# Optimization experiments

Hardware: AMD Instinct MI355X
Metric: run time of the kernel (lower is better)

## Reference

```python
import jax, jax.numpy as jnp
import numpy as np

B, T, N = 8, 100, 100000
MARGIN = 0.1
THRESHOLD = 0.5
BIG = 1.0e9


def setup_inputs() -> dict:
    key = jax.random.key(0)
    k0, k1, k2, k3, k4 = jax.random.split(key, 5)
    outputs = jax.random.normal(k0, (B, T, 3), dtype=jnp.float32)
    c2ws = jax.random.normal(k1, (B, 4, 4), dtype=jnp.float32)
    scene_scales = jax.random.uniform(k2, (B,), dtype=jnp.float32)
    means = jax.random.normal(k3, (N, 3), dtype=jnp.float32)
    scales = jax.random.uniform(k4, (N, 3), dtype=jnp.float32)
    return {"outputs": outputs, "c2ws": c2ws, "scene_scales": scene_scales,
            "means": means, "scales": scales}


def reference(outputs, c2ws, scene_scales, means, scales):
    # per-splat max radius (precomputed in torch __init__)
    maxsplatrad = jnp.max(scales, axis=1)                      # [N]
    # world transform: aff = R * scene_scale, trans = translation
    aff = c2ws[:, :3, :3] * scene_scales[:, None, None]        # [B,3,3]
    trans = c2ws[:, :3, 3]                                     # [B,3]
    # baddbmm(trans, outputs, aff.mT) == outputs @ aff^T + trans
    retrajs = jnp.einsum('btd,bed->bte', outputs, aff) + trans[:, None, :]  # [B,T,3]
    # axis-aligned bbox of each trajectory, expanded by threshold
    thres = THRESHOLD * scene_scales[0]
    uvals = jnp.max(retrajs, axis=1) + thres                   # [B,3]
    lvals = jnp.min(retrajs, axis=1) - thres                   # [B,3]
    # bbox filter: which splats fall inside each trajectory bbox
    inside = jnp.all((means[None, :, :] >= lvals[:, None, :]) &
                     (means[None, :, :] <= uvals[:, None, :]), axis=2)  # [B,N]
    # pairwise distances via ||a-b||^2 = |a|^2 + |b|^2 - 2 a.b (avoids [B,T,N,3])
    r2 = jnp.sum(retrajs * retrajs, axis=-1)                   # [B,T]
    m2 = jnp.sum(means * means, axis=-1)                       # [N]
    cross = jnp.einsum('btd,nd->btn', retrajs, means)          # [B,T,N]
    d2 = r2[:, :, None] + m2[None, None, :] - 2.0 * cross
    dist = jnp.sqrt(jnp.maximum(d2, 0.0))
    resdists = dist - maxsplatrad[None, None, :] - MARGIN      # [B,T,N]
    # scatter_reduce amin with include_self=False and 1e9 default ==
    # masked min over splats; pairs not inside bbox never scattered -> BIG
    masked = jnp.where(inside[:, None, :], resdists, BIG)
    collosses = jnp.min(masked, axis=2)                        # [B,T]
    return jnp.sum(jax.nn.relu(-collosses)) / (B * T)
```

## Files before the change

### kernel.cpp

```cpp
#include <hip/hip_runtime.h>

constexpr int   B_ = 8;
constexpr int   T_ = 100;
constexpr int   NPAIRS = B_ * T_;
constexpr int   N_ = 100000;
constexpr float MARGIN_ = 0.1f;
constexpr float THRESHOLD_ = 0.5f;
constexpr float BIG_ = 1000000000.0f;

constexpr size_t PM_OFF     = 0;
constexpr size_t MSR_OFF    = PM_OFF + (size_t)N_ * 16;
constexpr size_t KEYS_OFF   = MSR_OFF + (size_t)N_ * 32;
constexpr size_t PAIRS_OFF  = KEYS_OFF + 4096;
constexpr size_t BOUNDS_OFF = PAIRS_OFF + 16384;

__device__ __forceinline__ float fsqrt(float x) { return __builtin_amdgcn_sqrtf(x); }

__device__ __forceinline__ unsigned fkey(float f) {
    unsigned u = __float_as_uint(f);
    return (u & 0x80000000u) ? ~u : (u | 0x80000000u);
}

__global__ void k_prep(const float* __restrict__ outputs,
                       const float* __restrict__ c2ws,
                       const float* __restrict__ ss,
                       char* ws) {
    __shared__ float re_s[NPAIRS * 3];
    int tid = threadIdx.x;
    float4*   pairs  = (float4*)(ws + PAIRS_OFF);
    float*    bounds = (float*)(ws + BOUNDS_OFF);
    unsigned* keys   = (unsigned*)(ws + KEYS_OFF);

    if (tid < NPAIRS) {
        int b = tid / T_;
        float s = ss[b];
        const float* o = outputs + tid * 3;
        float o0 = o[0], o1 = o[1], o2 = o[2];
        const float* c = c2ws + b * 16;
        float re[3];
#pragma unroll
        for (int e = 0; e < 3; e++) {
            re[e] = (o0 * c[e * 4 + 0] + o1 * c[e * 4 + 1] + o2 * c[e * 4 + 2]) * s + c[e * 4 + 3];
            re_s[tid * 3 + e] = re[e];
        }
        pairs[tid] = make_float4(re[0], re[1], re[2], 0.f);
        keys[tid] = fkey(BIG_);
    }

    __syncthreads();
    if (tid < 24) {
        int b = tid / 3, e = tid - b * 3;
        float mx = -3.4e38f, mn = 3.4e38f;
        for (int t = 0; t < T_; t++) {
            float v = re_s[(b * T_ + t) * 3 + e];
            mx = fmaxf(mx, v);
            mn = fminf(mn, v);
        }
        float thres = THRESHOLD_ * ss[0];
        bounds[b * 3 + e]      = mn - thres;
        bounds[24 + b * 3 + e] = mx + thres;
    }
}

__global__ void k_means(const float* __restrict__ means,
                        const float* __restrict__ scales,
                        char* ws) {
    int n = blockIdx.x * blockDim.x + threadIdx.x;
    if (n >= N_) return;
    const float* bounds = (const float*)(ws + BOUNDS_OFF);
    float4* pm   = (float4*)(ws + PM_OFF);
    float4* msrv = (float4*)(ws + MSR_OFF);

    float mx = means[n * 3 + 0], my = means[n * 3 + 1], mz = means[n * 3 + 2];
    float msr = fmaxf(fmaxf(scales[n * 3 + 0], scales[n * 3 + 1]), scales[n * 3 + 2]) + MARGIN_;
    float eff[8];
#pragma unroll
    for (int b = 0; b < 8; b++) {
        bool in = (mx >= bounds[b * 3 + 0]) & (mx <= bounds[24 + b * 3 + 0]) &
                  (my >= bounds[b * 3 + 1]) & (my <= bounds[24 + b * 3 + 1]) &
                  (mz >= bounds[b * 3 + 2]) & (mz <= bounds[24 + b * 3 + 2]);
        eff[b] = in ? msr : -BIG_;
    }
    pm[n] = make_float4(mx, my, mz, 0.f);
    msrv[n * 2 + 0] = make_float4(eff[0], eff[1], eff[2], eff[3]);
    msrv[n * 2 + 1] = make_float4(eff[4], eff[5], eff[6], eff[7]);
}

constexpr int PER = 98;
constexpr int NBLK = (N_ + PER - 1) / PER;

__global__ __launch_bounds__(256) void k_main(const char* __restrict__ wsc, char* ws) {
    __shared__ float4 pm_s[PER];
    __shared__ float  msr_s[PER * 8];
    int tid = threadIdx.x;
    const float4* pmg   = (const float4*)(wsc + PM_OFF);
    const float4* msrg  = (const float4*)(wsc + MSR_OFF);
    const float4* pairs = (const float4*)(wsc + PAIRS_OFF);
    unsigned* keys = (unsigned*)(ws + KEYS_OFF);

    int base = blockIdx.x * PER;
    int cnt  = min(PER, N_ - base);

    if (tid < cnt) pm_s[tid] = pmg[base + tid];
    if (tid < 2 * cnt) ((float4*)msr_s)[tid] = msrg[2 * base + tid];

    int p0 = tid, p1 = tid + 256, p2 = tid + 512;
    float4 q0 = pairs[p0];
    float4 q1 = pairs[p1];
    float4 q2 = pairs[p2];
    int b0 = p0 / T_, b1 = p1 / T_, b2 = p2 / T_;

    __syncthreads();

    float mn0 = BIG_, mn1 = BIG_, mn2 = BIG_;
    const float*  mp = msr_s;
    const float4* sp = pm_s;
    for (int i = 0; i < cnt; i++) {
        float4 m = sp[i];
        float e0 = mp[b0], e1 = mp[b1], e2 = mp[b2];
        mp += 8;
        float dx, dy, dz, d2;
        dx = q0.x - m.x; dy = q0.y - m.y; dz = q0.z - m.z;
        d2 = fmaf(dz, dz, fmaf(dy, dy, dx * dx));
        mn0 = fminf(mn0, fsqrt(d2) - e0);
        dx = q1.x - m.x; dy = q1.y - m.y; dz = q1.z - m.z;
        d2 = fmaf(dz, dz, fmaf(dy, dy, dx * dx));
        mn1 = fminf(mn1, fsqrt(d2) - e1);
        dx = q2.x - m.x; dy = q2.y - m.y; dz = q2.z - m.z;
        d2 = fmaf(dz, dz, fmaf(dy, dy, dx * dx));
        mn2 = fminf(mn2, fsqrt(d2) - e2);
    }
    atomicMin(&keys[p0], fkey(mn0));
    atomicMin(&keys[p1], fkey(mn1));
    atomicMin(&keys[p2], fkey(mn2));

    if (tid < 32) {
        int p3 = 768 + tid;
        float4 q3 = pairs[p3];
        int b3 = p3 / T_;
        float mn3 = BIG_;
        const float* mp3 = msr_s;
        for (int i = 0; i < cnt; i++) {
            float4 m = pm_s[i];
            float e3 = mp3[b3];
            mp3 += 8;
            float dx = q3.x - m.x, dy = q3.y - m.y, dz = q3.z - m.z;
            float d2 = fmaf(dz, dz, fmaf(dy, dy, dx * dx));
            mn3 = fminf(mn3, fsqrt(d2) - e3);
        }
        atomicMin(&keys[p3], fkey(mn3));
    }
}

__global__ void k_final(const char* __restrict__ wsc, float* __restrict__ out) {
    const unsigned* keys = (const unsigned*)(wsc + KEYS_OFF);
    int tid = threadIdx.x;
    float acc = 0.f;
    for (int p = tid; p < NPAIRS; p += 256) {
        unsigned k = keys[p];
        unsigned u = (k & 0x80000000u) ? (k ^ 0x80000000u) : ~k;
        float f = __uint_as_float(u);
        acc += fmaxf(0.f, -f);
    }
#pragma unroll
    for (int off = 32; off; off >>= 1) acc += __shfl_down(acc, off, 64);
    __shared__ float wsum[4];
    if ((tid & 63) == 0) wsum[tid >> 6] = acc;
    __syncthreads();
    if (tid == 0) out[0] = (wsum[0] + wsum[1] + wsum[2] + wsum[3]) / (float)(B_ * T_);
}

extern "C" void kernel_launch(void* const* d_in, const int* in_sizes, int n_in,
                              void* d_out, int out_size, void* d_ws, size_t ws_size,
                              hipStream_t stream) {
    const float* outputs = (const float*)d_in[0];
    const float* c2ws    = (const float*)d_in[1];
    const float* ss      = (const float*)d_in[2];
    const float* means   = (const float*)d_in[3];
    const float* scales  = (const float*)d_in[4];
    float* out = (float*)d_out;
    char*  ws  = (char*)d_ws;

    hipLaunchKernelGGL(k_prep, dim3(1), dim3(1024), 0, stream, outputs, c2ws, ss, ws);
    hipLaunchKernelGGL(k_means, dim3((N_ + 255) / 256), dim3(256), 0, stream, means, scales, ws);
    hipLaunchKernelGGL(k_main, dim3(NBLK), dim3(256), 0, stream, (const char*)ws, ws);
    hipLaunchKernelGGL(k_final, dim3(1), dim3(256), 0, stream, (const char*)ws, out);
}
```

Before: 101.5 us.

## Fuse means preprocessing and final reduction into main kernel

Removes the separate per-splat preprocessing kernel by computing bbox masks and max radii directly into shared memory in the main kernel. Replaces the final reduction kernel with a last-block-done pattern using an atomic counter and threadfences. This cuts two kernel launches and the global round trip of the preprocessed splat arrays. The cost is an extra atomic and fence per block, plus redundant bound loads per thread.

```diff
diff --git a/kernel.cpp b/kernel.cpp
--- a/kernel.cpp
+++ b/kernel.cpp
@@ -8,11 +8,10 @@
 constexpr float THRESHOLD_ = 0.5f;
 constexpr float BIG_ = 1000000000.0f;
 
-constexpr size_t PM_OFF     = 0;
-constexpr size_t MSR_OFF    = PM_OFF + (size_t)N_ * 16;
-constexpr size_t KEYS_OFF   = MSR_OFF + (size_t)N_ * 32;
-constexpr size_t PAIRS_OFF  = KEYS_OFF + 4096;
-constexpr size_t BOUNDS_OFF = PAIRS_OFF + 16384;
+constexpr size_t PAIRS_OFF  = 0;
+constexpr size_t BOUNDS_OFF = 16384;
+constexpr size_t KEYS_OFF   = BOUNDS_OFF + 256;
+constexpr size_t CNT_OFF    = KEYS_OFF + NPAIRS * 4;
 
 __device__ __forceinline__ float fsqrt(float x) { return __builtin_amdgcn_sqrtf(x); }
 
@@ -30,6 +29,9 @@
     float4*   pairs  = (float4*)(ws + PAIRS_OFF);
     float*    bounds = (float*)(ws + BOUNDS_OFF);
     unsigned* keys   = (unsigned*)(ws + KEYS_OFF);
+    unsigned* cnt    = (unsigned*)(ws + CNT_OFF);
+
+    if (tid == 0) *cnt = 0;
 
     if (tid < NPAIRS) {
         int b = tid / T_;
@@ -44,7 +46,7 @@
             re_s[tid * 3 + e] = re[e];
         }
         pairs[tid] = make_float4(re[0], re[1], re[2], 0.f);
-        keys[tid] = fkey(BIG_);
+        keys[tid]  = fkey(BIG_);
     }
 
     __syncthreads();
@@ -62,47 +64,42 @@
     }
 }
 
-__global__ void k_means(const float* __restrict__ means,
-                        const float* __restrict__ scales,
-                        char* ws) {
-    int n = blockIdx.x * blockDim.x + threadIdx.x;
-    if (n >= N_) return;
-    const float* bounds = (const float*)(ws + BOUNDS_OFF);
-    float4* pm   = (float4*)(ws + PM_OFF);
-    float4* msrv = (float4*)(ws + MSR_OFF);
-
-    float mx = means[n * 3 + 0], my = means[n * 3 + 1], mz = means[n * 3 + 2];
-    float msr = fmaxf(fmaxf(scales[n * 3 + 0], scales[n * 3 + 1]), scales[n * 3 + 2]) + MARGIN_;
-    float eff[8];
-#pragma unroll
-    for (int b = 0; b < 8; b++) {
-        bool in = (mx >= bounds[b * 3 + 0]) & (mx <= bounds[24 + b * 3 + 0]) &
-                  (my >= bounds[b * 3 + 1]) & (my <= bounds[24 + b * 3 + 1]) &
-                  (mz >= bounds[b * 3 + 2]) & (mz <= bounds[24 + b * 3 + 2]);
-        eff[b] = in ? msr : -BIG_;
-    }
-    pm[n] = make_float4(mx, my, mz, 0.f);
-    msrv[n * 2 + 0] = make_float4(eff[0], eff[1], eff[2], eff[3]);
-    msrv[n * 2 + 1] = make_float4(eff[4], eff[5], eff[6], eff[7]);
-}
-
 constexpr int PER = 98;
 constexpr int NBLK = (N_ + PER - 1) / PER;
 
-__global__ __launch_bounds__(256) void k_main(const char* __restrict__ wsc, char* ws) {
+__global__ __launch_bounds__(256) void k_main(const float* __restrict__ means,
+                                              const float* __restrict__ scales,
+                                              const char* __restrict__ wsc, char* ws,
+                                              float* __restrict__ out) {
     __shared__ float4 pm_s[PER];
     __shared__ float  msr_s[PER * 8];
+    __shared__ int    isLast;
+    __shared__ float  wsum[4];
     int tid = threadIdx.x;
-    const float4* pmg   = (const float4*)(wsc + PM_OFF);
-    const float4* msrg  = (const float4*)(wsc + MSR_OFF);
-    const float4* pairs = (const float4*)(wsc + PAIRS_OFF);
+    const float4* pairs  = (const float4*)(wsc + PAIRS_OFF);
+    const float*  bounds = (const float*)(wsc + BOUNDS_OFF);
     unsigned* keys = (unsigned*)(ws + KEYS_OFF);
+    unsigned* cnt  = (unsigned*)(ws + CNT_OFF);
 
     int base = blockIdx.x * PER;
-    int cnt  = min(PER, N_ - base);
+    int cntn = min(PER, N_ - base);
 
-    if (tid < cnt) pm_s[tid] = pmg[base + tid];
-    if (tid < 2 * cnt) ((float4*)msr_s)[tid] = msrg[2 * base + tid];
+    if (tid < cntn) {
+        int n = base + tid;
+        float mx = means[(size_t)n * 3 + 0];
+        float my = means[(size_t)n * 3 + 1];
+        float mz = means[(size_t)n * 3 + 2];
+        float msr = fmaxf(fmaxf(scales[(size_t)n * 3 + 0], scales[(size_t)n * 3 + 1]),
+                          scales[(size_t)n * 3 + 2]) + MARGIN_;
+        pm_s[tid] = make_float4(mx, my, mz, 0.f);
+#pragma unroll
+        for (int b = 0; b < 8; b++) {
+            bool in = (mx >= bounds[b * 3 + 0]) & (mx <= bounds[24 + b * 3 + 0]) &
+                      (my >= bounds[b * 3 + 1]) & (my <= bounds[24 + b * 3 + 1]) &
+                      (mz >= bounds[b * 3 + 2]) & (mz <= bounds[24 + b * 3 + 2]);
+            msr_s[tid * 8 + b] = in ? msr : -BIG_;
+        }
+    }
 
     int p0 = tid, p1 = tid + 256, p2 = tid + 512;
     float4 q0 = pairs[p0];
@@ -115,7 +112,7 @@
     float mn0 = BIG_, mn1 = BIG_, mn2 = BIG_;
     const float*  mp = msr_s;
     const float4* sp = pm_s;
-    for (int i = 0; i < cnt; i++) {
+    for (int i = 0; i < cntn; i++) {
         float4 m = sp[i];
         float e0 = mp[b0], e1 = mp[b1], e2 = mp[b2];
         mp += 8;
@@ -140,7 +137,7 @@
         int b3 = p3 / T_;
         float mn3 = BIG_;
         const float* mp3 = msr_s;
-        for (int i = 0; i < cnt; i++) {
+        for (int i = 0; i < cntn; i++) {
             float4 m = pm_s[i];
             float e3 = mp3[b3];
             mp3 += 8;
@@ -150,24 +147,28 @@
         }
         atomicMin(&keys[p3], fkey(mn3));
     }
-}
 
-__global__ void k_final(const char* __restrict__ wsc, float* __restrict__ out) {
-    const unsigned* keys = (const unsigned*)(wsc + KEYS_OFF);
-    int tid = threadIdx.x;
-    float acc = 0.f;
-    for (int p = tid; p < NPAIRS; p += 256) {
-        unsigned k = keys[p];
-        unsigned u = (k & 0x80000000u) ? (k ^ 0x80000000u) : ~k;
-        float f = __uint_as_float(u);
-        acc += fmaxf(0.f, -f);
+    __threadfence();
+    if (tid == 0) {
+        unsigned prev = atomicAdd(cnt, 1u);
+        isLast = (prev == (unsigned)(NBLK - 1));
     }
+    __syncthreads();
+    if (isLast) {
+        __threadfence();
+        float acc = 0.f;
+        for (int p = tid; p < NPAIRS; p += 256) {
+            unsigned k = __hip_atomic_load(&keys[p], __ATOMIC_RELAXED, __HIP_MEMORY_SCOPE_AGENT);
+            unsigned u = (k & 0x80000000u) ? (k ^ 0x80000000u) : ~k;
+            float f = __uint_as_float(u);
+            acc += fmaxf(0.f, -f);
+        }
 #pragma unroll
-    for (int off = 32; off; off >>= 1) acc += __shfl_down(acc, off, 64);
-    __shared__ float wsum[4];
-    if ((tid & 63) == 0) wsum[tid >> 6] = acc;
-    __syncthreads();
-    if (tid == 0) out[0] = (wsum[0] + wsum[1] + wsum[2] + wsum[3]) / (float)(B_ * T_);
+        for (int off = 32; off; off >>= 1) acc += __shfl_down(acc, off, 64);
+        if ((tid & 63) == 0) wsum[tid >> 6] = acc;
+        __syncthreads();
+        if (tid == 0) out[0] = (wsum[0] + wsum[1] + wsum[2] + wsum[3]) / (float)(B_ * T_);
+    }
 }
 
 extern "C" void kernel_launch(void* const* d_in, const int* in_sizes, int n_in,
@@ -182,7 +183,6 @@
     char*  ws  = (char*)d_ws;
 
     hipLaunchKernelGGL(k_prep, dim3(1), dim3(1024), 0, stream, outputs, c2ws, ss, ws);
-    hipLaunchKernelGGL(k_means, dim3((N_ + 255) / 256), dim3(256), 0, stream, means, scales, ws);
-    hipLaunchKernelGGL(k_main, dim3(NBLK), dim3(256), 0, stream, (const char*)ws, ws);
-    hipLaunchKernelGGL(k_final, dim3(1), dim3(256), 0, stream, (const char*)ws, out);
+    hipLaunchKernelGGL(k_main, dim3(NBLK), dim3(256), 0, stream,
+                       means, scales, (const char*)ws, ws, out);
 }
```

Result: slower. 136.9 us (+34.8%).
